# Performance work log

Measured on AMD Instinct MI355X. Metric: run time of the kernel, lower is better.

## Reference

```python
import jax, jax.numpy as jnp
import numpy as np

B, T, I, H, O = 32, 512, 128, 1024, 128


def _lstm_layer(xs, W_ih, W_hh, b):
    """xs: [B, T, D_in] -> hidden sequence [B, T, H]. Torch LSTM cell math."""
    # Precompute all input projections in one big GEMM: [B, T, 4H]
    x_proj = jnp.einsum('btd,gd->btg', xs, W_ih) + b
    x_proj = jnp.transpose(x_proj, (1, 0, 2))  # time-major [T, B, 4H]
    h0 = jnp.zeros((xs.shape[0], H), xs.dtype)
    c0 = jnp.zeros((xs.shape[0], H), xs.dtype)

    def step(carry, xp):
        h, c = carry
        gates = xp + h @ W_hh.T  # [B, 4H]
        i, f, g, o = jnp.split(gates, 4, axis=-1)
        i = jax.nn.sigmoid(i)
        f = jax.nn.sigmoid(f)
        g = jnp.tanh(g)
        o = jax.nn.sigmoid(o)
        c = f * c + i * g
        h = o * jnp.tanh(c)
        return (h, c), h

    _, hs = jax.lax.scan(step, (h0, c0), x_proj)  # hs: [T, B, H]
    return jnp.transpose(hs, (1, 0, 2))  # [B, T, H]


def setup_inputs() -> dict:
    key = jax.random.key(0)
    ks = jax.random.split(key, 9)
    s_ih0 = 1.0 / np.sqrt(I)
    s_h = 1.0 / np.sqrt(H)
    return {
        'state': jax.random.normal(ks[0], (B, T, I), jnp.float32),
        'W_ih_0': jax.random.normal(ks[1], (4 * H, I), jnp.float32) * s_ih0,
        'W_hh_0': jax.random.normal(ks[2], (4 * H, H), jnp.float32) * s_h,
        'b_0': jax.random.normal(ks[3], (4 * H,), jnp.float32) * s_h,
        'W_ih_1': jax.random.normal(ks[4], (4 * H, H), jnp.float32) * s_h,
        'W_hh_1': jax.random.normal(ks[5], (4 * H, H), jnp.float32) * s_h,
        'b_1': jax.random.normal(ks[6], (4 * H,), jnp.float32) * s_h,
        'W_out': jax.random.normal(ks[7], (O, H), jnp.float32) * s_h,
        'b_out': jax.random.normal(ks[8], (O,), jnp.float32) * s_h,
    }


def reference(state, W_ih_0, W_hh_0, b_0, W_ih_1, W_hh_1, b_1, W_out, b_out):
    h1 = _lstm_layer(state, W_ih_0, W_hh_0, b_0)   # [B, T, H]
    h2 = _lstm_layer(h1, W_ih_1, W_hh_1, b_1)      # [B, T, H]
    # per-timestep linear head, as in the per-step loop of the original
    out = jnp.einsum('bth,oh->bto', h2, W_out) + b_out  # [B, T, O]
    return out
```

## Files before the change

kernel.cpp:

```cpp
#include <hip/hip_runtime.h>

#define NB 32
#define NT 512
#define NI 128
#define NH 1024
#define NG 4096
#define NO 128

typedef _Float16 f16;
typedef _Float16 f16x8 __attribute__((ext_vector_type(8)));
typedef float f32x4 __attribute__((ext_vector_type(4)));
typedef int int4v __attribute__((ext_vector_type(4)));
typedef unsigned long long ull;

#define MFMA16(a, b, c) __builtin_amdgcn_mfma_f32_16x16x32_f16(a, b, c, 0, 0, 0)
#define SENTD 0x7F7F7F7Fu

__device__ __forceinline__ float sigm(float x) { return 1.f / (1.f + __expf(-x)); }
__device__ __forceinline__ float tanh_(float x) {
    float a = fabsf(x);
    float e = __expf(-2.f * a);
    float r = (1.f - e) / (1.f + e);
    return x < 0.f ? -r : r;
}
__device__ __forceinline__ bool ok16(int4v v) {
    return v.x != (int)SENTD && v.y != (int)SENTD && v.z != (int)SENTD && v.w != (int)SENTD;
}
__device__ __forceinline__ void astore64(void* p, ull v) {
    __hip_atomic_store((ull*)p, v, __ATOMIC_RELAXED, __HIP_MEMORY_SCOPE_AGENT);
}
__device__ __forceinline__ f16x8 ld8f(const float* s) {
    float4 x0 = *(const float4*)s, x1 = *(const float4*)(s + 4);
    f16x8 v;
    v[0] = (f16)x0.x; v[1] = (f16)x0.y; v[2] = (f16)x0.z; v[3] = (f16)x0.w;
    v[4] = (f16)x1.x; v[5] = (f16)x1.y; v[6] = (f16)x1.z; v[7] = (f16)x1.w;
    return v;
}
#define LOAD_SC01(dst, addr) \
    asm volatile("global_load_dwordx4 %0, %1, off sc0 sc1" : "=v"(dst) : "v"(addr))
#define WAITV0() do { asm volatile("s_waitcnt vmcnt(0)" ::: "memory"); \
                      __builtin_amdgcn_sched_barrier(0); } while (0)

__global__ void convf16(const float* __restrict__ src, f16* __restrict__ dst, int n) {
    int i = blockIdx.x * blockDim.x + threadIdx.x;
    if (i < n) dst[i] = (f16)src[i];
}

extern "C" __global__ __launch_bounds__(256, 1) void persist(
    const float* __restrict__ Wih0f, const float* __restrict__ Whh0f, const float* __restrict__ b0,
    const float* __restrict__ Wih1f, const float* __restrict__ Whh1f, const float* __restrict__ b1,
    const f16* __restrict__ state16,
    f16* __restrict__ h1all,
    f16* __restrict__ h2all)
{
    extern __shared__ char smem[];
    float* gbuf = (float*)smem;
    const int bid = blockIdx.x;
    const int tid = threadIdx.x;
    const int w = tid >> 6;
    const int lane = tid & 63;
    const int llo = lane & 15;
    const int lhi = lane >> 4;
    const int rb = tid >> 2;
    const int uq = (tid & 3) * 4;

    if (bid < 128) {
        const int bs = bid >> 6, us = bid & 63;
        const int bbase = bs * 16, ubase = us * 16;
        f16x8 wr[36];
#pragma unroll
        for (int g = 0; g < 4; ++g)
#pragma unroll
            for (int i = 0; i < 9; ++i) {
                int kpos = (w * 9 + i) * 32 + lhi * 8;
                int col = g * NH + ubase + llo;
                const float* s = (kpos < 128) ? (Wih0f + (size_t)col * NI + kpos)
                                              : (Whh0f + (size_t)col * NH + (kpos - 128));
                wr[g * 9 + i] = ld8f(s);
            }
        float cc[4] = {0.f, 0.f, 0.f, 0.f};
        float Bi[4], Bff[4], Bg[4], Bo[4];
        if (tid < 64) {
#pragma unroll
            for (int u = 0; u < 4; ++u) {
                Bi[u]  = b0[0 * NH + ubase + uq + u];
                Bff[u] = b0[1 * NH + ubase + uq + u];
                Bg[u]  = b0[2 * NH + ubase + uq + u];
                Bo[u]  = b0[3 * NH + ubase + uq + u];
            }
        }

        for (int t = 0; t < NT; ++t) {
            const f16* hprev = h1all + (size_t)(t - 1) * NB * NH;
            const int row = bbase + llo;
            int4v vv[9];
#pragma unroll
            for (int i = 0; i < 9; ++i) {
                int kpos = (w * 9 + i) * 32 + lhi * 8;
                if (kpos < 128)
                    vv[i] = *(const int4v*)(state16 + ((size_t)row * NT + t) * NI + kpos);
                else if (t > 0) {
                    LOAD_SC01(vv[i], hprev + (size_t)row * NH + (kpos - 128));
                } else
                    vv[i] = int4v{};
            }
            if (t > 0) {
                WAITV0();
                unsigned pend = 0;
#pragma unroll
                for (int i = 0; i < 9; ++i) {
                    int kpos = (w * 9 + i) * 32 + lhi * 8;
                    if (kpos >= 128 && !ok16(vv[i])) pend |= 1u << i;
                }
                while (__builtin_expect(pend != 0, 0)) {
#pragma unroll
                    for (int i = 0; i < 9; ++i)
                        if (pend & (1u << i)) {
                            int kpos = (w * 9 + i) * 32 + lhi * 8;
                            LOAD_SC01(vv[i], hprev + (size_t)row * NH + (kpos - 128));
                        }
                    WAITV0();
#pragma unroll
                    for (int i = 0; i < 9; ++i)
                        if ((pend & (1u << i)) && ok16(vv[i])) pend &= ~(1u << i);
                    if (pend) __builtin_amdgcn_s_sleep(1);
                }
            }
            f32x4 acc[4] = {};
#pragma unroll
            for (int i = 0; i < 9; ++i) {
                f16x8 av = __builtin_bit_cast(f16x8, vv[i]);
#pragma unroll
                for (int g = 0; g < 4; ++g)
                    acc[g] = MFMA16(av, wr[g * 9 + i], acc[g]);
            }
            __syncthreads();
#pragma unroll
            for (int g = 0; g < 4; ++g)
#pragma unroll
                for (int r = 0; r < 4; ++r)
                    gbuf[(w * 4 + g) * 272 + (lhi * 4 + r) * 17 + llo] = acc[g][r];
            __syncthreads();
            if (tid < 64) {
                ull pack = 0;
#pragma unroll
                for (int u = 0; u < 4; ++u) {
                    int un = uq + u;
                    float s0 = 0, s1 = 0, s2 = 0, s3 = 0;
#pragma unroll
                    for (int w2 = 0; w2 < 4; ++w2) {
                        s0 += gbuf[(w2 * 4 + 0) * 272 + rb * 17 + un];
                        s1 += gbuf[(w2 * 4 + 1) * 272 + rb * 17 + un];
                        s2 += gbuf[(w2 * 4 + 2) * 272 + rb * 17 + un];
                        s3 += gbuf[(w2 * 4 + 3) * 272 + rb * 17 + un];
                    }
                    float i_ = sigm(s0 + Bi[u]), f_ = sigm(s1 + Bff[u]);
                    float g_ = tanh_(s2 + Bg[u]), o_ = sigm(s3 + Bo[u]);
                    cc[u] = f_ * cc[u] + i_ * g_;
                    float h = o_ * tanh_(cc[u]);
                    unsigned short hb = __builtin_bit_cast(unsigned short, (f16)h);
                    pack |= (ull)hb << (16 * u);
                }
                astore64(h1all + ((size_t)t * NB + bbase + rb) * NH + ubase + uq, pack);
            }
        }
    } else {
        const int b2 = bid - 128, bs = b2 >> 6, us = b2 & 63;
        const int bbase = bs * 16, ubase = us * 16;
        f16x8 wr1[32], wr2[32];
#pragma unroll
        for (int g = 0; g < 4; ++g)
#pragma unroll
            for (int i = 0; i < 8; ++i) {
                int kpos = (w * 8 + i) * 32 + lhi * 8;
                int col = g * NH + ubase + llo;
                wr1[g * 8 + i] = ld8f(Wih1f + (size_t)col * NH + kpos);
                wr2[g * 8 + i] = ld8f(Whh1f + (size_t)col * NH + kpos);
            }
        float cc[4] = {0.f, 0.f, 0.f, 0.f};
        float Bi[4], Bff[4], Bg[4], Bo[4];
        if (tid < 64) {
#pragma unroll
            for (int u = 0; u < 4; ++u) {
                Bi[u]  = b1[0 * NH + ubase + uq + u];
                Bff[u] = b1[1 * NH + ubase + uq + u];
                Bg[u]  = b1[2 * NH + ubase + uq + u];
                Bo[u]  = b1[3 * NH + ubase + uq + u];
            }
        }
        const int row = bbase + llo;

        for (int t = 0; t < NT; ++t) {
            const f16* A1 = h1all + (size_t)t * NB * NH;
            const f16* A2 = h2all + (size_t)(t - 1) * NB * NH;
            int4v v1[8], v2[8];
#pragma unroll
            for (int i = 0; i < 8; ++i) {
                int kpos = (w * 8 + i) * 32 + lhi * 8;
                LOAD_SC01(v1[i], A1 + (size_t)row * NH + kpos);
            }
            if (t > 0) {
#pragma unroll
                for (int i = 0; i < 8; ++i) {
                    int kpos = (w * 8 + i) * 32 + lhi * 8;
                    LOAD_SC01(v2[i], A2 + (size_t)row * NH + kpos);
                }
            } else {
#pragma unroll
                for (int i = 0; i < 8; ++i) v2[i] = int4v{};
            }
            WAITV0();
            unsigned p1 = 0, p2 = 0;
#pragma unroll
            for (int i = 0; i < 8; ++i) {
                if (!ok16(v1[i])) p1 |= 1u << i;
                if (t > 0 && !ok16(v2[i])) p2 |= 1u << i;
            }
            while (__builtin_expect((p1 | p2) != 0, 0)) {
#pragma unroll
                for (int i = 0; i < 8; ++i) {
                    int kpos = (w * 8 + i) * 32 + lhi * 8;
                    if (p1 & (1u << i)) LOAD_SC01(v1[i], A1 + (size_t)row * NH + kpos);
                    if (p2 & (1u << i)) LOAD_SC01(v2[i], A2 + (size_t)row * NH + kpos);
                }
                WAITV0();
#pragma unroll
                for (int i = 0; i < 8; ++i) {
                    if ((p1 & (1u << i)) && ok16(v1[i])) p1 &= ~(1u << i);
                    if ((p2 & (1u << i)) && ok16(v2[i])) p2 &= ~(1u << i);
                }
                if (p1 | p2) __builtin_amdgcn_s_sleep(1);
            }

            f32x4 acc[4] = {};
#pragma unroll
            for (int i = 0; i < 8; ++i) {
                f16x8 a1 = __builtin_bit_cast(f16x8, v1[i]);
                f16x8 a2 = __builtin_bit_cast(f16x8, v2[i]);
#pragma unroll
                for (int g = 0; g < 4; ++g) {
                    acc[g] = MFMA16(a1, wr1[g * 8 + i], acc[g]);
                    acc[g] = MFMA16(a2, wr2[g * 8 + i], acc[g]);
                }
            }
            __syncthreads();
#pragma unroll
            for (int g = 0; g < 4; ++g)
#pragma unroll
                for (int r = 0; r < 4; ++r)
                    gbuf[(w * 4 + g) * 272 + (lhi * 4 + r) * 17 + llo] = acc[g][r];
            __syncthreads();
            if (tid < 64) {
                ull pack = 0;
#pragma unroll
                for (int u = 0; u < 4; ++u) {
                    int un = uq + u;
                    float s0 = 0, s1 = 0, s2 = 0, s3 = 0;
#pragma unroll
                    for (int w2 = 0; w2 < 4; ++w2) {
                        s0 += gbuf[(w2 * 4 + 0) * 272 + rb * 17 + un];
                        s1 += gbuf[(w2 * 4 + 1) * 272 + rb * 17 + un];
                        s2 += gbuf[(w2 * 4 + 2) * 272 + rb * 17 + un];
                        s3 += gbuf[(w2 * 4 + 3) * 272 + rb * 17 + un];
                    }
                    float i_ = sigm(s0 + Bi[u]), f_ = sigm(s1 + Bff[u]);
                    float g_ = tanh_(s2 + Bg[u]), o_ = sigm(s3 + Bo[u]);
                    cc[u] = f_ * cc[u] + i_ * g_;
                    float h = o_ * tanh_(cc[u]);
                    unsigned short hb = __builtin_bit_cast(unsigned short, (f16)h);
                    pack |= (ull)hb << (16 * u);
                }
                astore64(h2all + ((size_t)t * NB + bbase + rb) * NH + ubase + uq, pack);
            }
        }
    }
}

__device__ __forceinline__ void stage_h(const f16* __restrict__ hsrc, char* smem, int tid) {
    const float4* src = (const float4*)hsrc;
#pragma unroll
    for (int i = 0; i < 16; ++i) {
        int c = i * 256 + tid;
        int off = c * 16;
        int swz = off ^ (((off >> 11) & 7) << 4);
        *(float4*)(smem + swz) = src[c];
    }
}
__device__ __forceinline__ f16x8 afrag(const char* smem, int row, int kk) {
    int off = (row << 11) + kk * 2;
    off ^= ((row & 7) << 4);
    return *(const f16x8*)(smem + off);
}

__global__ __launch_bounds__(256) void head_kernel(
    const f16* __restrict__ h2all, const f16* __restrict__ Wout,
    const float* __restrict__ bout, float* __restrict__ out)
{
    __shared__ __align__(16) char smem[65536];
    int t = blockIdx.x;
    int tid = threadIdx.x;
    int wave = tid >> 6, lane = tid & 63, lhi = lane >> 4, llo = lane & 15;
    stage_h(h2all + (size_t)t * NB * NH, smem, tid);
    __syncthreads();

    f32x4 acc[2][2];
#pragma unroll
    for (int nt = 0; nt < 2; ++nt) {
        int col = wave * 32 + nt * 16 + llo;
        float bb = bout[col];
#pragma unroll
        for (int r = 0; r < 4; ++r) { acc[0][nt][r] = bb; acc[1][nt][r] = bb; }
    }
#pragma unroll 8
    for (int kt = 0; kt < 32; ++kt) {
        int kk = kt * 32 + lhi * 8;
        f16x8 a0 = afrag(smem, llo, kk);
        f16x8 a1 = afrag(smem, 16 + llo, kk);
#pragma unroll
        for (int nt = 0; nt < 2; ++nt) {
            int col = wave * 32 + nt * 16 + llo;
            f16x8 bf = *(const f16x8*)(Wout + (size_t)col * NH + kk);
            acc[0][nt] = MFMA16(a0, bf, acc[0][nt]);
            acc[1][nt] = MFMA16(a1, bf, acc[1][nt]);
        }
    }
#pragma unroll
    for (int nt = 0; nt < 2; ++nt) {
        int col = wave * 32 + nt * 16 + llo;
#pragma unroll
        for (int r = 0; r < 4; ++r) {
            out[(size_t)(lhi * 4 + r) * NT * NO + (size_t)t * NO + col] = acc[0][nt][r];
            out[(size_t)(16 + lhi * 4 + r) * NT * NO + (size_t)t * NO + col] = acc[1][nt][r];
        }
    }
}

extern "C" void kernel_launch(void* const* d_in, const int* in_sizes, int n_in,
                              void* d_out, int out_size, void* d_ws, size_t ws_size,
                              hipStream_t stream)
{
    const float* state = (const float*)d_in[0];
    const float* Wih0f = (const float*)d_in[1];
    const float* Whh0f = (const float*)d_in[2];
    const float* b0    = (const float*)d_in[3];
    const float* Wih1f = (const float*)d_in[4];
    const float* Whh1f = (const float*)d_in[5];
    const float* b1    = (const float*)d_in[6];
    const float* Woutf = (const float*)d_in[7];
    const float* bout  = (const float*)d_in[8];
    float* out = (float*)d_out;
    (void)in_sizes; (void)n_in; (void)out_size; (void)ws_size;

    size_t off = 0;
    char* base = (char*)d_ws;
    auto alloc = [&](size_t bytes) -> void* {
        void* p = base + off;
        off += (bytes + 255) & ~(size_t)255;
        return p;
    };
    f16* state16 = (f16*)alloc((size_t)NB * NT * NI * 2);
    f16* Wout    = (f16*)alloc((size_t)NO * NH * 2);
    f16* h1all   = (f16*)alloc((size_t)NT * NB * NH * 2);
    f16* h2all   = (f16*)alloc((size_t)NT * NB * NH * 2);

    convf16<<<(NB * NT * NI + 255) / 256, 256, 0, stream>>>(state, state16, NB * NT * NI);
    convf16<<<(NO * NH + 255) / 256, 256, 0, stream>>>(Woutf, Wout, NO * NH);
    hipMemsetAsync(h1all, 0x7F, (size_t)2 * NT * NB * NH * 2, stream);

    hipFuncSetAttribute((const void*)persist,
                        hipFuncAttributeMaxDynamicSharedMemorySize, 86016);
    persist<<<256, 256, 86016, stream>>>(Wih0f, Whh0f, b0, Wih1f, Whh1f, b1,
                                         state16, h1all, h2all);
    head_kernel<<<NT, 256, 0, stream>>>(h2all, Wout, bout, out);
}
```

Measured before the change: 2.986 ms.

## Replace sentinel-polling of hidden states with per-block ready flags

Adds per-timestep, per-block flag arrays that each block sets after writing its slice of h, so consumers poll 64 flags with one wavefront instead of spinning on sentinel values inside the full hidden-state loads. After the flag wait and a block barrier, h is read with ordinary cached loads. This is meant to cut the cost of repeated sc0/sc1 uncached vector loads and retry loops on the recurrent critical path. In exchange it adds a release barrier, an extra flag store, and a flag poll plus a block-wide sync every step. The sentinel check is still kept as a fallback, and ordering relies on relaxed atomics plus waitcnt, which could be a visibility risk.

```diff
diff --git a/kernel.cpp b/kernel.cpp
--- a/kernel.cpp
+++ b/kernel.cpp
@@ -29,6 +29,9 @@
 __device__ __forceinline__ void astore64(void* p, ull v) {
     __hip_atomic_store((ull*)p, v, __ATOMIC_RELAXED, __HIP_MEMORY_SCOPE_AGENT);
 }
+__device__ __forceinline__ void astore32u(void* p, unsigned v) {
+    __hip_atomic_store((unsigned*)p, v, __ATOMIC_RELAXED, __HIP_MEMORY_SCOPE_AGENT);
+}
 __device__ __forceinline__ f16x8 ld8f(const float* s) {
     float4 x0 = *(const float4*)s, x1 = *(const float4*)(s + 4);
     f16x8 v;
@@ -38,6 +41,8 @@
 }
 #define LOAD_SC01(dst, addr) \
     asm volatile("global_load_dwordx4 %0, %1, off sc0 sc1" : "=v"(dst) : "v"(addr))
+#define LOAD_DW_SC01(dst, addr) \
+    asm volatile("global_load_dword %0, %1, off sc0 sc1" : "=v"(dst) : "v"(addr))
 #define WAITV0() do { asm volatile("s_waitcnt vmcnt(0)" ::: "memory"); \
                       __builtin_amdgcn_sched_barrier(0); } while (0)
 
@@ -51,7 +56,9 @@
     const float* __restrict__ Wih1f, const float* __restrict__ Whh1f, const float* __restrict__ b1,
     const f16* __restrict__ state16,
     f16* __restrict__ h1all,
-    f16* __restrict__ h2all)
+    f16* __restrict__ h2all,
+    unsigned* __restrict__ flags1,
+    unsigned* __restrict__ flags2)
 {
     extern __shared__ char smem[];
     float* gbuf = (float*)smem;
@@ -93,19 +100,30 @@
         for (int t = 0; t < NT; ++t) {
             const f16* hprev = h1all + (size_t)(t - 1) * NB * NH;
             const int row = bbase + llo;
+            if (t > 0) {
+                if (w == 0) {
+                    const unsigned* fp = flags1 + (size_t)(t - 1) * 128 + bs * 64 + lane;
+                    int r = 0;
+                    for (;;) {
+                        unsigned v; LOAD_DW_SC01(v, fp); WAITV0();
+                        if (__all(v != 0)) break;
+                        if (++r > 8) __builtin_amdgcn_s_sleep(1);
+                    }
+                }
+                __syncthreads();
+            }
             int4v vv[9];
 #pragma unroll
             for (int i = 0; i < 9; ++i) {
                 int kpos = (w * 9 + i) * 32 + lhi * 8;
                 if (kpos < 128)
                     vv[i] = *(const int4v*)(state16 + ((size_t)row * NT + t) * NI + kpos);
-                else if (t > 0) {
-                    LOAD_SC01(vv[i], hprev + (size_t)row * NH + (kpos - 128));
-                } else
+                else if (t > 0)
+                    vv[i] = *(const int4v*)(hprev + (size_t)row * NH + (kpos - 128));
+                else
                     vv[i] = int4v{};
             }
             if (t > 0) {
-                WAITV0();
                 unsigned pend = 0;
 #pragma unroll
                 for (int i = 0; i < 9; ++i) {
@@ -163,6 +181,9 @@
                 }
                 astore64(h1all + ((size_t)t * NB + bbase + rb) * NH + ubase + uq, pack);
             }
+            WAITV0();
+            __syncthreads();
+            if (tid == 0) astore32u(flags1 + (size_t)t * 128 + bid, 1u);
         }
     } else {
         const int b2 = bid - 128, bs = b2 >> 6, us = b2 & 63;
@@ -193,23 +214,40 @@
         for (int t = 0; t < NT; ++t) {
             const f16* A1 = h1all + (size_t)t * NB * NH;
             const f16* A2 = h2all + (size_t)(t - 1) * NB * NH;
+            if (w == 0) {
+                const unsigned* fp = flags1 + (size_t)t * 128 + bs * 64 + lane;
+                int r = 0;
+                for (;;) {
+                    unsigned v; LOAD_DW_SC01(v, fp); WAITV0();
+                    if (__all(v != 0)) break;
+                    if (++r > 8) __builtin_amdgcn_s_sleep(1);
+                }
+            } else if (w == 1 && t > 0) {
+                const unsigned* fp = flags2 + (size_t)(t - 1) * 128 + bs * 64 + lane;
+                int r = 0;
+                for (;;) {
+                    unsigned v; LOAD_DW_SC01(v, fp); WAITV0();
+                    if (__all(v != 0)) break;
+                    if (++r > 8) __builtin_amdgcn_s_sleep(1);
+                }
+            }
+            __syncthreads();
             int4v v1[8], v2[8];
 #pragma unroll
             for (int i = 0; i < 8; ++i) {
                 int kpos = (w * 8 + i) * 32 + lhi * 8;
-                LOAD_SC01(v1[i], A1 + (size_t)row * NH + kpos);
+                v1[i] = *(const int4v*)(A1 + (size_t)row * NH + kpos);
             }
             if (t > 0) {
 #pragma unroll
                 for (int i = 0; i < 8; ++i) {
                     int kpos = (w * 8 + i) * 32 + lhi * 8;
-                    LOAD_SC01(v2[i], A2 + (size_t)row * NH + kpos);
+                    v2[i] = *(const int4v*)(A2 + (size_t)row * NH + kpos);
                 }
             } else {
 #pragma unroll
                 for (int i = 0; i < 8; ++i) v2[i] = int4v{};
             }
-            WAITV0();
             unsigned p1 = 0, p2 = 0;
 #pragma unroll
             for (int i = 0; i < 8; ++i) {
@@ -272,6 +310,9 @@
                 }
                 astore64(h2all + ((size_t)t * NB + bbase + rb) * NH + ubase + uq, pack);
             }
+            WAITV0();
+            __syncthreads();
+            if (tid == 0) astore32u(flags2 + (size_t)t * 128 + b2, 1u);
         }
     }
 }
@@ -362,14 +403,17 @@
     f16* Wout    = (f16*)alloc((size_t)NO * NH * 2);
     f16* h1all   = (f16*)alloc((size_t)NT * NB * NH * 2);
     f16* h2all   = (f16*)alloc((size_t)NT * NB * NH * 2);
+    unsigned* flags1 = (unsigned*)alloc((size_t)NT * 128 * 4);
+    unsigned* flags2 = (unsigned*)alloc((size_t)NT * 128 * 4);
 
     convf16<<<(NB * NT * NI + 255) / 256, 256, 0, stream>>>(state, state16, NB * NT * NI);
     convf16<<<(NO * NH + 255) / 256, 256, 0, stream>>>(Woutf, Wout, NO * NH);
     hipMemsetAsync(h1all, 0x7F, (size_t)2 * NT * NB * NH * 2, stream);
+    hipMemsetAsync(flags1, 0, (size_t)2 * NT * 128 * 4, stream);
 
     hipFuncSetAttribute((const void*)persist,
                         hipFuncAttributeMaxDynamicSharedMemorySize, 86016);
     persist<<<256, 256, 86016, stream>>>(Wih0f, Whh0f, b0, Wih1f, Whh1f, b1,
-                                         state16, h1all, h2all);
+                                         state16, h1all, h2all, flags1, flags2);
     head_kernel<<<NT, 256, 0, stream>>>(h2all, Wout, bout, out);
 }
```

Result: slower. 3.547 ms (+18.8%).

## Prefetch next-step recurrent loads early and split gate epilogue across two waves

Applied to the files above, without the earlier changes.

The loads for the next timestep (the input slice plus the previous hidden state in layer 0, and the own-layer previous hidden state in layer 1) are now issued at the end of the current step. Their latency can then overlap the loop back-edge and, in layer 1, the h1 load, instead of starting after the previous step finishes. The pointwise LSTM epilogue is spread over 128 threads handling 2 units each with 32-bit atomic stores, instead of 64 threads handling 4 units, which shortens the serial tail of each step. The risk is that early-issued hidden-state loads more often read sentinel values and fall into the retry loop, and the stores are now narrower and more numerous.

```diff
diff --git a/kernel.cpp b/kernel.cpp
--- a/kernel.cpp
+++ b/kernel.cpp
@@ -26,8 +26,8 @@
 __device__ __forceinline__ bool ok16(int4v v) {
     return v.x != (int)SENTD && v.y != (int)SENTD && v.z != (int)SENTD && v.w != (int)SENTD;
 }
-__device__ __forceinline__ void astore64(void* p, ull v) {
-    __hip_atomic_store((ull*)p, v, __ATOMIC_RELAXED, __HIP_MEMORY_SCOPE_AGENT);
+__device__ __forceinline__ void astore32u(void* p, unsigned v) {
+    __hip_atomic_store((unsigned*)p, v, __ATOMIC_RELAXED, __HIP_MEMORY_SCOPE_AGENT);
 }
 __device__ __forceinline__ f16x8 ld8f(const float* s) {
     float4 x0 = *(const float4*)s, x1 = *(const float4*)(s + 4);
@@ -61,12 +61,13 @@
     const int lane = tid & 63;
     const int llo = lane & 15;
     const int lhi = lane >> 4;
-    const int rb = tid >> 2;
-    const int uq = (tid & 3) * 4;
+    const int eb = tid >> 3;
+    const int up = (tid & 7) * 2;
 
     if (bid < 128) {
         const int bs = bid >> 6, us = bid & 63;
         const int bbase = bs * 16, ubase = us * 16;
+        const int row = bbase + llo;
         f16x8 wr[36];
 #pragma unroll
         for (int g = 0; g < 4; ++g)
@@ -78,34 +79,38 @@
                                               : (Whh0f + (size_t)col * NH + (kpos - 128));
                 wr[g * 9 + i] = ld8f(s);
             }
-        float cc[4] = {0.f, 0.f, 0.f, 0.f};
-        float Bi[4], Bff[4], Bg[4], Bo[4];
-        if (tid < 64) {
-#pragma unroll
-            for (int u = 0; u < 4; ++u) {
-                Bi[u]  = b0[0 * NH + ubase + uq + u];
-                Bff[u] = b0[1 * NH + ubase + uq + u];
-                Bg[u]  = b0[2 * NH + ubase + uq + u];
-                Bo[u]  = b0[3 * NH + ubase + uq + u];
-            }
-        }
-
-        for (int t = 0; t < NT; ++t) {
-            const f16* hprev = h1all + (size_t)(t - 1) * NB * NH;
-            const int row = bbase + llo;
-            int4v vv[9];
+        float cc2[2] = {0.f, 0.f};
+        float Bi[2], Bff[2], Bg[2], Bo[2];
+        if (tid < 128) {
+#pragma unroll
+            for (int j = 0; j < 2; ++j) {
+                Bi[j]  = b0[0 * NH + ubase + up + j];
+                Bff[j] = b0[1 * NH + ubase + up + j];
+                Bg[j]  = b0[2 * NH + ubase + up + j];
+                Bo[j]  = b0[3 * NH + ubase + up + j];
+            }
+        }
+
+        int4v vv[9];
+        auto issue1 = [&](int tn) {
 #pragma unroll
             for (int i = 0; i < 9; ++i) {
                 int kpos = (w * 9 + i) * 32 + lhi * 8;
                 if (kpos < 128)
-                    vv[i] = *(const int4v*)(state16 + ((size_t)row * NT + t) * NI + kpos);
-                else if (t > 0) {
-                    LOAD_SC01(vv[i], hprev + (size_t)row * NH + (kpos - 128));
+                    vv[i] = *(const int4v*)(state16 + ((size_t)row * NT + tn) * NI + kpos);
+                else if (tn > 0) {
+                    LOAD_SC01(vv[i], h1all + (size_t)(tn - 1) * NB * NH
+                                     + (size_t)row * NH + (kpos - 128));
                 } else
                     vv[i] = int4v{};
             }
+        };
+        issue1(0);
+
+        for (int t = 0; t < NT; ++t) {
+            const f16* hprev = h1all + (size_t)(t - 1) * NB * NH;
+            WAITV0();
             if (t > 0) {
-                WAITV0();
                 unsigned pend = 0;
 #pragma unroll
                 for (int i = 0; i < 9; ++i) {
@@ -141,32 +146,34 @@
                 for (int r = 0; r < 4; ++r)
                     gbuf[(w * 4 + g) * 272 + (lhi * 4 + r) * 17 + llo] = acc[g][r];
             __syncthreads();
-            if (tid < 64) {
-                ull pack = 0;
-#pragma unroll
-                for (int u = 0; u < 4; ++u) {
-                    int un = uq + u;
+            if (tid < 128) {
+                unsigned pk = 0;
+#pragma unroll
+                for (int j = 0; j < 2; ++j) {
+                    int un = up + j;
                     float s0 = 0, s1 = 0, s2 = 0, s3 = 0;
 #pragma unroll
                     for (int w2 = 0; w2 < 4; ++w2) {
-                        s0 += gbuf[(w2 * 4 + 0) * 272 + rb * 17 + un];
-                        s1 += gbuf[(w2 * 4 + 1) * 272 + rb * 17 + un];
-                        s2 += gbuf[(w2 * 4 + 2) * 272 + rb * 17 + un];
-                        s3 += gbuf[(w2 * 4 + 3) * 272 + rb * 17 + un];
+                        s0 += gbuf[(w2 * 4 + 0) * 272 + eb * 17 + un];
+                        s1 += gbuf[(w2 * 4 + 1) * 272 + eb * 17 + un];
+                        s2 += gbuf[(w2 * 4 + 2) * 272 + eb * 17 + un];
+                        s3 += gbuf[(w2 * 4 + 3) * 272 + eb * 17 + un];
                     }
-                    float i_ = sigm(s0 + Bi[u]), f_ = sigm(s1 + Bff[u]);
-                    float g_ = tanh_(s2 + Bg[u]), o_ = sigm(s3 + Bo[u]);
-                    cc[u] = f_ * cc[u] + i_ * g_;
-                    float h = o_ * tanh_(cc[u]);
+                    float i_ = sigm(s0 + Bi[j]), f_ = sigm(s1 + Bff[j]);
+                    float g_ = tanh_(s2 + Bg[j]), o_ = sigm(s3 + Bo[j]);
+                    cc2[j] = f_ * cc2[j] + i_ * g_;
+                    float h = o_ * tanh_(cc2[j]);
                     unsigned short hb = __builtin_bit_cast(unsigned short, (f16)h);
-                    pack |= (ull)hb << (16 * u);
-                }
-                astore64(h1all + ((size_t)t * NB + bbase + rb) * NH + ubase + uq, pack);
-            }
+                    pk |= (unsigned)hb << (16 * j);
+                }
+                astore32u(h1all + ((size_t)t * NB + bbase + eb) * NH + ubase + up, pk);
+            }
+            if (t + 1 < NT) issue1(t + 1);
         }
     } else {
         const int b2 = bid - 128, bs = b2 >> 6, us = b2 & 63;
         const int bbase = bs * 16, ubase = us * 16;
+        const int row = bbase + llo;
         f16x8 wr1[32], wr2[32];
 #pragma unroll
         for (int g = 0; g < 4; ++g)
@@ -177,37 +184,39 @@
                 wr1[g * 8 + i] = ld8f(Wih1f + (size_t)col * NH + kpos);
                 wr2[g * 8 + i] = ld8f(Whh1f + (size_t)col * NH + kpos);
             }
-        float cc[4] = {0.f, 0.f, 0.f, 0.f};
-        float Bi[4], Bff[4], Bg[4], Bo[4];
-        if (tid < 64) {
-#pragma unroll
-            for (int u = 0; u < 4; ++u) {
-                Bi[u]  = b1[0 * NH + ubase + uq + u];
-                Bff[u] = b1[1 * NH + ubase + uq + u];
-                Bg[u]  = b1[2 * NH + ubase + uq + u];
-                Bo[u]  = b1[3 * NH + ubase + uq + u];
-            }
-        }
-        const int row = bbase + llo;
+        float cc2[2] = {0.f, 0.f};
+        float Bi[2], Bff[2], Bg[2], Bo[2];
+        if (tid < 128) {
+#pragma unroll
+            for (int j = 0; j < 2; ++j) {
+                Bi[j]  = b1[0 * NH + ubase + up + j];
+                Bff[j] = b1[1 * NH + ubase + up + j];
+                Bg[j]  = b1[2 * NH + ubase + up + j];
+                Bo[j]  = b1[3 * NH + ubase + up + j];
+            }
+        }
+
+        int4v v1[8], v2[8];
+        auto issueV2 = [&](int tn) {
+#pragma unroll
+            for (int i = 0; i < 8; ++i) {
+                int kpos = (w * 8 + i) * 32 + lhi * 8;
+                if (tn > 0) {
+                    LOAD_SC01(v2[i], h2all + (size_t)(tn - 1) * NB * NH
+                                     + (size_t)row * NH + kpos);
+                } else
+                    v2[i] = int4v{};
+            }
+        };
+        issueV2(0);
 
         for (int t = 0; t < NT; ++t) {
             const f16* A1 = h1all + (size_t)t * NB * NH;
             const f16* A2 = h2all + (size_t)(t - 1) * NB * NH;
-            int4v v1[8], v2[8];
 #pragma unroll
             for (int i = 0; i < 8; ++i) {
                 int kpos = (w * 8 + i) * 32 + lhi * 8;
                 LOAD_SC01(v1[i], A1 + (size_t)row * NH + kpos);
-            }
-            if (t > 0) {
-#pragma unroll
-                for (int i = 0; i < 8; ++i) {
-                    int kpos = (w * 8 + i) * 32 + lhi * 8;
-                    LOAD_SC01(v2[i], A2 + (size_t)row * NH + kpos);
-                }
-            } else {
-#pragma unroll
-                for (int i = 0; i < 8; ++i) v2[i] = int4v{};
             }
             WAITV0();
             unsigned p1 = 0, p2 = 0;
@@ -250,28 +259,29 @@
                 for (int r = 0; r < 4; ++r)
                     gbuf[(w * 4 + g) * 272 + (lhi * 4 + r) * 17 + llo] = acc[g][r];
             __syncthreads();
-            if (tid < 64) {
-                ull pack = 0;
-#pragma unroll
-                for (int u = 0; u < 4; ++u) {
-                    int un = uq + u;
+            if (tid < 128) {
+                unsigned pk = 0;
+#pragma unroll
+                for (int j = 0; j < 2; ++j) {
+                    int un = up + j;
                     float s0 = 0, s1 = 0, s2 = 0, s3 = 0;
 #pragma unroll
                     for (int w2 = 0; w2 < 4; ++w2) {
-                        s0 += gbuf[(w2 * 4 + 0) * 272 + rb * 17 + un];
-                        s1 += gbuf[(w2 * 4 + 1) * 272 + rb * 17 + un];
-                        s2 += gbuf[(w2 * 4 + 2) * 272 + rb * 17 + un];
-                        s3 += gbuf[(w2 * 4 + 3) * 272 + rb * 17 + un];
+                        s0 += gbuf[(w2 * 4 + 0) * 272 + eb * 17 + un];
+                        s1 += gbuf[(w2 * 4 + 1) * 272 + eb * 17 + un];
+                        s2 += gbuf[(w2 * 4 + 2) * 272 + eb * 17 + un];
+                        s3 += gbuf[(w2 * 4 + 3) * 272 + eb * 17 + un];
                     }
-                    float i_ = sigm(s0 + Bi[u]), f_ = sigm(s1 + Bff[u]);
-                    float g_ = tanh_(s2 + Bg[u]), o_ = sigm(s3 + Bo[u]);
-                    cc[u] = f_ * cc[u] + i_ * g_;
-                    float h = o_ * tanh_(cc[u]);
+                    float i_ = sigm(s0 + Bi[j]), f_ = sigm(s1 + Bff[j]);
+                    float g_ = tanh_(s2 + Bg[j]), o_ = sigm(s3 + Bo[j]);
+                    cc2[j] = f_ * cc2[j] + i_ * g_;
+                    float h = o_ * tanh_(cc2[j]);
                     unsigned short hb = __builtin_bit_cast(unsigned short, (f16)h);
-                    pack |= (ull)hb << (16 * u);
-                }
-                astore64(h2all + ((size_t)t * NB + bbase + rb) * NH + ubase + uq, pack);
-            }
+                    pk |= (unsigned)hb << (16 * j);
+                }
+                astore32u(h2all + ((size_t)t * NB + bbase + eb) * NH + ubase + up, pk);
+            }
+            if (t + 1 < NT) issueV2(t + 1);
         }
     }
 }
```

Result: slower. 3.208 ms (+7.4%).
